# Performance work log

Measured on AMD Instinct MI355X. Metric: run time of the kernel, lower is better.

Reference implementation:

```python
import jax, jax.numpy as jnp
import numpy as np
import math

N, DIM, HEADS = 4096, 128, 8
HC = DIM // HEADS      # MHA per-head dim = 16
GC = DIM               # TransformerConv per-head out_channels = dim (concat=False)
E = 65536
FFN = 2048
EPS = 1e-5

def layernorm(x, g, b):
    m = x.mean(-1, keepdims=True)
    v = ((x - m) ** 2).mean(-1, keepdims=True)
    return (x - m) * jax.lax.rsqrt(v + EPS) * g + b

def setup_inputs() -> dict:
    key = jax.random.key(0)
    ks = jax.random.split(key, 24)
    s = 0.02
    def nrm(k, shape):
        return jax.random.normal(k, shape, jnp.float32) * s
    return dict(
        x=jax.random.normal(ks[0], (N, DIM), jnp.float32),
        edge_index=jax.random.randint(ks[1], (2, E), 0, N),
        edge_attr=jax.random.normal(ks[2], (E, DIM), jnp.float32),
        n1_g=jnp.ones((DIM,)), n1_b=jnp.zeros((DIM,)),
        n2_g=jnp.ones((DIM,)), n2_b=jnp.zeros((DIM,)),
        n3_g=jnp.ones((DIM,)), n3_b=jnp.zeros((DIM,)),
        w_qkv=nrm(ks[3], (DIM, 3 * DIM)), b_qkv=jnp.zeros((3 * DIM,)),
        w_o=nrm(ks[4], (DIM, DIM)), b_o=jnp.zeros((DIM,)),
        w_query=nrm(ks[5], (DIM, HEADS * GC)), b_query=jnp.zeros((HEADS * GC,)),
        w_key=nrm(ks[6], (DIM, HEADS * GC)), b_key=jnp.zeros((HEADS * GC,)),
        w_value=nrm(ks[7], (DIM, HEADS * GC)), b_value=jnp.zeros((HEADS * GC,)),
        w_edge=nrm(ks[8], (DIM, HEADS * GC)), b_edge=jnp.zeros((HEADS * GC,)),
        w_skip=nrm(ks[9], (DIM, GC)), b_skip=jnp.zeros((GC,)),
        w_beta=nrm(ks[10], (3 * GC, 1)),
        w_f1=nrm(ks[11], (DIM, FFN)), b_f1=jnp.zeros((FFN,)),
        w_f2=nrm(ks[12], (FFN, DIM)), b_f2=jnp.zeros((DIM,)),
        w_dyn=nrm(ks[13], (2 * DIM, DIM)), b_dyn=jnp.zeros((DIM,)),
    )

def reference(x, edge_index, edge_attr, n1_g, n1_b, n2_g, n2_b, n3_g, n3_b,
              w_qkv, b_qkv, w_o, b_o,
              w_query, b_query, w_key, b_key, w_value, b_value,
              w_edge, b_edge, w_skip, b_skip, w_beta,
              w_f1, b_f1, w_f2, b_f2, w_dyn, b_dyn):
    residual = x
    xn = layernorm(x, n1_g, n1_b)
    # ---- dense self-attention (batch 1, batch_first MHA, eval mode) ----
    qkv = xn @ w_qkv + b_qkv
    q, k, v = jnp.split(qkv, 3, axis=-1)
    q = q.reshape(N, HEADS, HC)
    k = k.reshape(N, HEADS, HC)
    v = v.reshape(N, HEADS, HC)
    scores = jnp.einsum('qhd,khd->hqk', q, k) / math.sqrt(HC)
    probs = jax.nn.softmax(scores, axis=-1)
    attn = jnp.einsum('hqk,khd->qhd', probs, v).reshape(N, DIM)
    attn = attn @ w_o + b_o
    x = residual + attn
    # ---- TransformerConv (heads=8, concat=False -> mean, beta=True, edge_dim=dim) ----
    xn2 = layernorm(x, n2_g, n2_b)
    src, dst = edge_index[0], edge_index[1]   # source -> target flow
    qg = (xn2 @ w_query + b_query).reshape(N, HEADS, GC)
    kg = (xn2 @ w_key + b_key).reshape(N, HEADS, GC)
    vg = (xn2 @ w_value + b_value).reshape(N, HEADS, GC)
    eg = (edge_attr @ w_edge + b_edge).reshape(E, HEADS, GC)
    kj = kg[src] + eg                          # key_j + edge embedding
    alpha = jnp.einsum('ehd,ehd->eh', qg[dst], kj) / math.sqrt(GC)  # [E,H]
    amax = jax.ops.segment_max(alpha, dst, num_segments=N)          # [N,H]
    amax = jnp.where(jnp.isfinite(amax), amax, 0.0)
    ea = jnp.exp(alpha - amax[dst])
    denom = jax.ops.segment_sum(ea, dst, num_segments=N)
    w = ea / (denom[dst] + 1e-16)              # segment softmax per target node
    msg = (vg[src] + eg) * w[:, :, None]       # value_j + edge, scaled
    agg = jax.ops.segment_sum(msg, dst, num_segments=N)  # [N,H,GC]
    out = agg.mean(axis=1)                     # concat=False -> head mean
    x_r = xn2 @ w_skip + b_skip                # root/skip path
    beta = jax.nn.sigmoid(jnp.concatenate([out, x_r, out - x_r], axis=-1) @ w_beta)
    graph_out = beta * x_r + (1.0 - beta) * out
    x = x + graph_out
    # ---- FFN ----
    xn3 = layernorm(x, n3_g, n3_b)
    ffn = jax.nn.gelu(xn3 @ w_f1 + b_f1, approximate=False) @ w_f2 + b_f2
    x = x + ffn
    # ---- gated residual fusion ----
    gate = jax.nn.sigmoid(jnp.concatenate([x, residual], axis=-1) @ w_dyn + b_dyn)
    return x * gate + residual * (1.0 - gate)
```

## Files before the change

### kernel.cpp

```cpp
#include <hip/hip_runtime.h>
#include <math.h>
#include <cstddef>

#define NN 4096
#define DIMC 128
#define NHEADS 8
#define NE 65536

typedef unsigned short ushort_t;
typedef short bs8 __attribute__((ext_vector_type(8)));
typedef float f32x16 __attribute__((ext_vector_type(16)));
typedef _Float16 h4 __attribute__((ext_vector_type(4)));
typedef __fp16 fp16x2 __attribute__((ext_vector_type(2)));
typedef float f4t __attribute__((ext_vector_type(4)));

__device__ __forceinline__ float b2f(ushort_t u){
  unsigned int i = ((unsigned int)u)<<16; float f;
  __builtin_memcpy(&f,&i,4); return f;
}
__device__ __forceinline__ ushort_t f2b(float f){
  unsigned int x; __builtin_memcpy(&x,&f,4);
  unsigned int r = x + 0x7fffu + ((x>>16)&1u);
  return (ushort_t)(r>>16);
}
__device__ __forceinline__ float bdot8(uint4 a, uint4 b){
  unsigned int ua[4]={a.x,a.y,a.z,a.w}, ub[4]={b.x,b.y,b.z,b.w};
  float s=0.f;
  #pragma unroll
  for (int i=0;i<4;++i){
    unsigned int al=ua[i]<<16, ah=ua[i]&0xffff0000u, bl=ub[i]<<16, bh=ub[i]&0xffff0000u;
    float fa,fb,fc,fd;
    __builtin_memcpy(&fa,&al,4); __builtin_memcpy(&fb,&ah,4);
    __builtin_memcpy(&fc,&bl,4); __builtin_memcpy(&fd,&bh,4);
    s += fa*fc + fb*fd;
  }
  return s;
}
__device__ __forceinline__ float bfdot8v(uint4 a, float4 e0, float4 e1){
  unsigned int ua[4]={a.x,a.y,a.z,a.w};
  float eb[8]={e0.x,e0.y,e0.z,e0.w,e1.x,e1.y,e1.z,e1.w};
  float s=0.f;
  #pragma unroll
  for (int i=0;i<4;++i){
    unsigned int al=ua[i]<<16, ah=ua[i]&0xffff0000u;
    float fa,fb;
    __builtin_memcpy(&fa,&al,4); __builtin_memcpy(&fb,&ah,4);
    s += fa*eb[2*i] + fb*eb[2*i+1];
  }
  return s;
}

__global__ __launch_bounds__(256) void ln_kernel(const float* __restrict__ x,
    const float* __restrict__ g, const float* __restrict__ b, ushort_t* __restrict__ y){
  int n = blockIdx.x*4 + (threadIdx.x>>6);
  int l = threadIdx.x & 63;
  int d0 = 2*l;
  float2 v = *(const float2*)&x[(size_t)n*DIMC + d0];
  float s = v.x+v.y;
  s += __shfl_xor(s,1); s += __shfl_xor(s,2); s += __shfl_xor(s,4);
  s += __shfl_xor(s,8); s += __shfl_xor(s,16); s += __shfl_xor(s,32);
  float mean = s*(1.0f/128.0f);
  float c0=v.x-mean, c1=v.y-mean;
  float q=c0*c0+c1*c1;
  q += __shfl_xor(q,1); q += __shfl_xor(q,2); q += __shfl_xor(q,4);
  q += __shfl_xor(q,8); q += __shfl_xor(q,16); q += __shfl_xor(q,32);
  float rinv = rsqrtf(q*(1.0f/128.0f)+1e-5f);
  float2 gv = *(const float2*)&g[d0];
  float2 bv = *(const float2*)&b[d0];
  unsigned int pk = ((unsigned int)f2b(c1*rinv*gv.y+bv.y)<<16) | (unsigned int)f2b(c0*rinv*gv.x+bv.x);
  *(unsigned int*)&y[(size_t)n*DIMC + d0] = pk;
}

#define QSCALE 0.36067376022224085f
__global__ __launch_bounds__(256) void megawcvt_kernel(
    const float* __restrict__ w_qkv, const float* __restrict__ w_o,
    const float* __restrict__ w_q, const float* __restrict__ w_k,
    const float* __restrict__ w_v, const float* __restrict__ w_e,
    const float* __restrict__ w_f1, const float* __restrict__ w_f2,
    const float* __restrict__ bq, const float* __restrict__ bk,
    const float* __restrict__ w_dyn, const float* __restrict__ b_qkv,
    ushort_t* __restrict__ WBqkv, ushort_t* __restrict__ WBo, ushort_t* __restrict__ WBG,
    ushort_t* __restrict__ WETB, ushort_t* __restrict__ WBf1, ushort_t* __restrict__ WBf2,
    ushort_t* __restrict__ WCAT, float* __restrict__ BCAT, ushort_t* __restrict__ WDYN,
    int* __restrict__ COUNT, float* __restrict__ BQKV)
{
  int b = blockIdx.x, tid = threadIdx.x;
  if (b < 1216){
    const float* src; int srcStride; ushort_t* dst; int dstStride;
    int n0, k0; float scale = 1.0f;
    if (b < 48){ int nt=b>>2, kt=b&3; src=w_qkv; srcStride=384; dst=WBqkv; dstStride=128;
      n0=nt*32; k0=kt*32; if (nt<4) scale=QSCALE; }
    else if (b < 64){ int l=b-48, nt=l>>2, kt=l&3; src=w_o; srcStride=128; dst=WBo; dstStride=128; n0=nt*32; k0=kt*32; }
    else if (b < 192){ int l=b-64, nt=l>>2, kt=l&3; src=w_q; srcStride=1024; dst=WBG; dstStride=128; n0=nt*32; k0=kt*32; }
    else if (b < 320){ int l=b-192, nt=l>>2, kt=l&3; src=w_k; srcStride=1024; dst=WBG+1024*128; dstStride=128; n0=nt*32; k0=kt*32; }
    else if (b < 448){ int l=b-320, nt=l>>2, kt=l&3; src=w_e; srcStride=1024; dst=WETB; dstStride=128; n0=nt*32; k0=kt*32; }
    else if (b < 704){ int l=b-448, nt=l>>2, kt=l&3; src=w_f1; srcStride=2048; dst=WBf1; dstStride=128; n0=nt*32; k0=kt*32; }
    else if (b < 960){ int l=b-704, nt=l>>6, kt=l&63; src=w_f2; srcStride=128; dst=WBf2; dstStride=2048; n0=nt*32; k0=kt*32; }
    else if (b < 1088){ int l=b-960, h=l>>4, tt=l&15, nt=tt>>2, kt=tt&3;
      src=w_v+h*128; srcStride=1024; dst=WCAT+h*128; dstStride=2048; n0=nt*32; k0=kt*32; scale=0.125f; }
    else { int l=b-1088, h=l>>4, tt=l&15, nt=tt>>2, kt=tt&3;
      src=w_e+h*128; srcStride=1024; dst=WCAT+1024+h*128; dstStride=2048; n0=nt*32; k0=kt*32; scale=0.125f; }
    __shared__ float lt[32*33];
    int rr = tid>>3, cg = (tid&7)*4;
    float4 v = *(const float4*)&src[(size_t)(k0+rr)*srcStride + n0 + cg];
    lt[rr*33+cg]=v.x; lt[rr*33+cg+1]=v.y; lt[rr*33+cg+2]=v.z; lt[rr*33+cg+3]=v.w;
    __syncthreads();
    ushort_t o[4] __attribute__((aligned(8)));
    #pragma unroll
    for (int j=0;j<4;++j) o[j] = f2b(lt[(cg+j)*33 + rr]*scale);
    *(ushort4*)&dst[(size_t)(n0+rr)*dstStride + k0 + cg] = *(ushort4*)o;
  } else {
    for (int id=(b-1216)*256+tid; id<39296; id += 40*256){
      if (id < 2048) BCAT[id] = (id<1024)? bq[id] : bk[id-1024];
      else if (id < 34816){ int l=id-2048; WDYN[l]=f2b(w_dyn[l]); }
      else if (id < 38912) COUNT[id-34816]=0;
      else { int l=id-38912; BQKV[l]=b_qkv[l]*((l<128)?QSCALE:1.0f); }
    }
  }
}

template<int A_BF16, int C_MODE>
__global__ __launch_bounds__(256) void mgemm_kernel(
    const void* __restrict__ Av, int lda, int strideA,
    const ushort_t* __restrict__ BT, int ldbt, int strideB,
    const float* __restrict__ bias,
    const float* __restrict__ res,
    void* __restrict__ Cv, int ldc, int strideC,
    int K, int act_gelu, _Float16* __restrict__ vtout)
{
  int z = blockIdx.z;
  int m0 = blockIdx.y*128, n0 = blockIdx.x*64;
  int tid = threadIdx.x;
  int w = tid>>6, lane = tid&63;
  int kg = lane>>5;
  int ml = w*32 + (lane&31);
  int sw = (ml>>1)&3;
  __shared__ ushort_t As[128*32];
  const ushort_t* BTz = BT + (size_t)z*strideB;
  f32x16 acc[2];
  #pragma unroll
  for (int i=0;i<16;++i){ acc[0][i]=0.f; acc[1][i]=0.f; }

  for (int k0=0; k0<K; k0+=32){
    {
      int rr = tid>>1, kc = (tid&1)*16;
      int rowg = m0 + rr;
      ushort_t tmp[16] __attribute__((aligned(16)));
      if (A_BF16){
        const ushort_t* A = (const ushort_t*)Av + (size_t)z*strideA;
        uint4 u0 = *(const uint4*)&A[(size_t)rowg*lda + k0 + kc];
        uint4 u1 = *(const uint4*)&A[(size_t)rowg*lda + k0 + kc + 8];
        __builtin_memcpy(tmp, &u0, 16); __builtin_memcpy(tmp+8, &u1, 16);
      } else {
        const float* A = (const float*)Av + (size_t)z*strideA;
        const float* p = &A[(size_t)rowg*lda + k0 + kc];
        float4 f0=*(const float4*)p, f1=*(const float4*)(p+4);
        float4 f2v=*(const float4*)(p+8), f3=*(const float4*)(p+12);
        tmp[0]=f2b(f0.x); tmp[1]=f2b(f0.y); tmp[2]=f2b(f0.z); tmp[3]=f2b(f0.w);
        tmp[4]=f2b(f1.x); tmp[5]=f2b(f1.y); tmp[6]=f2b(f1.z); tmp[7]=f2b(f1.w);
        tmp[8]=f2b(f2v.x); tmp[9]=f2b(f2v.y); tmp[10]=f2b(f2v.z); tmp[11]=f2b(f2v.w);
        tmp[12]=f2b(f3.x); tmp[13]=f2b(f3.y); tmp[14]=f2b(f3.z); tmp[15]=f2b(f3.w);
      }
      int swr = (rr>>1)&3, c0 = kc>>3;
      *(uint4*)&As[rr*32 + (((c0  )^swr)*8)] = *(const uint4*)tmp;
      *(uint4*)&As[rr*32 + (((c0+1)^swr)*8)] = *(const uint4*)(tmp+8);
    }
    __syncthreads();
    bs8 a0 = *(bs8*)&As[ml*32 + (((0*2+kg)^sw)*8)];
    bs8 a1 = *(bs8*)&As[ml*32 + (((1*2+kg)^sw)*8)];
    #pragma unroll
    for (int nt=0; nt<2; ++nt){
      const ushort_t* bp = &BTz[(size_t)(n0 + nt*32 + (lane&31))*ldbt + k0 + kg*8];
      uint4 rb0 = *(const uint4*)bp;
      uint4 rb1 = *(const uint4*)(bp + 16);
      bs8 b0, b1;
      __builtin_memcpy(&b0, &rb0, 16); __builtin_memcpy(&b1, &rb1, 16);
      acc[nt] = __builtin_amdgcn_mfma_f32_32x32x16_bf16(a0, b0, acc[nt], 0,0,0);
      acc[nt] = __builtin_amdgcn_mfma_f32_32x32x16_bf16(a1, b1, acc[nt], 0,0,0);
    }
    __syncthreads();
  }
  #pragma unroll
  for (int nt=0; nt<2; ++nt){
    int col = n0 + nt*32 + (lane&31);
    float bv = bias ? bias[col] : 0.f;
    #pragma unroll
    for (int r=0; r<16; ++r){
      int rowl = (r&3) + 8*(r>>2) + 4*kg;
      int row = m0 + w*32 + rowl;
      float v = acc[nt][r] + bv;
      if (act_gelu) v = 0.5f*v*(1.0f+erff(v*0.70710678118654752f));
      if (res) v += res[(size_t)row*ldc + col];
      size_t idx = (size_t)z*strideC + (size_t)row*ldc + col;
      if (C_MODE==1)      ((ushort_t*)Cv)[idx] = f2b(v);
      else if (C_MODE==2){
        _Float16 hv = (_Float16)v;
        ((_Float16*)Cv)[idx] = hv;
        if (vtout && col>=256) vtout[(size_t)(col-256)*4096 + row] = hv;
      }
      else                ((float*)Cv)[idx]    = v;
    }
  }
}

__global__ __launch_bounds__(512) void flash_kernel(const _Float16* __restrict__ qkvh,
    const _Float16* __restrict__ vt, float* __restrict__ attn){
  int h = blockIdx.y;
  int w = threadIdx.x >> 6, lane = threadIdx.x & 63;
  int q0 = blockIdx.x*64;
  int col = lane & 15, quad = lane >> 4;
  __shared__ float ll[8][4][16];
  __shared__ float lo[8][4][256];
  h4 qf[4];
  #pragma unroll
  for (int t=0;t<4;++t)
    qf[t] = *(const h4*)&qkvh[(size_t)(q0+t*16+col)*384 + h*16 + quad*4];
  f4t ov[4];
  float ls[4] = {0.f,0.f,0.f,0.f};
  #pragma unroll
  for (int t=0;t<4;++t){ ov[t][0]=0.f; ov[t][1]=0.f; ov[t][2]=0.f; ov[t][3]=0.f; }
  const _Float16* kbase = qkvh + 128 + h*16 + quad*4;
  const _Float16* vbase = vt + (size_t)(h*16+col)*4096 + quad*4;
  int jbeg = w*512, jend = jbeg + 512;
  h4 kf = *(const h4*)&kbase[(size_t)(jbeg+col)*384];
  h4 vf = *(const h4*)&vbase[jbeg];
  for (int j0=jbeg; j0<jend; j0+=16){
    h4 kc=kf, vc=vf;
    if (j0+16<jend){
      kf = *(const h4*)&kbase[(size_t)(j0+16+col)*384];
      vf = *(const h4*)&vbase[j0+16];
    }
    f4t s[4];
    #pragma unroll
    for (int t=0;t<4;++t){
      s[t][0]=0.f; s[t][1]=0.f; s[t][2]=0.f; s[t][3]=0.f;
      s[t] = __builtin_amdgcn_mfma_f32_16x16x16f16(kc, qf[t], s[t], 0,0,0);
    }
    #pragma unroll
    for (int t=0;t<4;++t){
      float p0=__builtin_amdgcn_exp2f(s[t][0]), p1=__builtin_amdgcn_exp2f(s[t][1]);
      float p2=__builtin_amdgcn_exp2f(s[t][2]), p3=__builtin_amdgcn_exp2f(s[t][3]);
      ls[t] += (p0+p1)+(p2+p3);
      fp16x2 plo = __builtin_amdgcn_cvt_pkrtz(p0,p1);
      fp16x2 phi = __builtin_amdgcn_cvt_pkrtz(p2,p3);
      h4 pf;
      pf[0]=(_Float16)plo[0]; pf[1]=(_Float16)plo[1];
      pf[2]=(_Float16)phi[0]; pf[3]=(_Float16)phi[1];
      ov[t] = __builtin_amdgcn_mfma_f32_16x16x16f16(vc, pf, ov[t], 0,0,0);
    }
  }
  #pragma unroll
  for (int t=0;t<4;++t){
    float l = ls[t];
    l += __shfl_xor(l,16);
    l += __shfl_xor(l,32);
    if (lane<16) ll[w][t][lane]=l;
    *(float4*)&lo[w][t][lane*4] = make_float4(ov[t][0],ov[t][1],ov[t][2],ov[t][3]);
  }
  __syncthreads();
  if (w < 4){
    int t = w;
    float l = 0.f;
    #pragma unroll
    for (int ww=0; ww<8; ++ww) l += ll[ww][t][col];
    float4 os = make_float4(0.f,0.f,0.f,0.f);
    #pragma unroll
    for (int ww=0; ww<8; ++ww){
      float4 owv = *(const float4*)&lo[ww][t][lane*4];
      os.x += owv.x; os.y += owv.y; os.z += owv.z; os.w += owv.w;
    }
    float inv = 1.0f/l;
    *(float4*)&attn[(size_t)(q0+t*16+col)*128 + h*16 + quad*4] =
        make_float4(os.x*inv, os.y*inv, os.z*inv, os.w*inv);
  }
}

__global__ __launch_bounds__(256) void alpha_kernel(
    const float* __restrict__ ea, const ushort_t* __restrict__ qkvsg,
    const ushort_t* __restrict__ t, const int* __restrict__ csr,
    const int* __restrict__ pack, float* __restrict__ alpha){
  int tid = threadIdx.x;
  int w = tid>>6, lane = tid&63;
  int h = lane>>3, li = lane&7;
  int off = h*128 + li*16;
  int ibase = blockIdx.x*8 + w*2;
  int2 pk = *(const int2*)&pack[ibase];
  int2 ec = *(const int2*)&csr[ibase];
  int e0 = ec.x & (NE-1), e1 = ec.y & (NE-1);
  int s0 = pk.x & 4095, d0 = (pk.x>>12) & 4095;
  int s1 = pk.y & 4095, d1 = (pk.y>>12) & 4095;

  const ushort_t* q0p = &qkvsg[(size_t)d0*2048 + off];
  const ushort_t* k0p = &qkvsg[(size_t)s0*2048 + 1024 + off];
  const ushort_t* t0p = &t[(size_t)d0*1024 + off];
  const float*    e0p = &ea[(size_t)e0*128 + li*16];
  const ushort_t* q1p = &qkvsg[(size_t)d1*2048 + off];
  const ushort_t* k1p = &qkvsg[(size_t)s1*2048 + 1024 + off];
  const ushort_t* t1p = &t[(size_t)d1*1024 + off];
  const float*    e1p = &ea[(size_t)e1*128 + li*16];

  uint4 q00=*(const uint4*)q0p,      q01=*(const uint4*)(q0p+8);
  uint4 k00=*(const uint4*)k0p,      k01=*(const uint4*)(k0p+8);
  uint4 t00=*(const uint4*)t0p,      t01=*(const uint4*)(t0p+8);
  float4 ea00=*(const float4*)e0p,   ea01=*(const float4*)(e0p+4);
  float4 ea02=*(const float4*)(e0p+8), ea03=*(const float4*)(e0p+12);
  uint4 q10=*(const uint4*)q1p,      q11=*(const uint4*)(q1p+8);
  uint4 k10=*(const uint4*)k1p,      k11=*(const uint4*)(k1p+8);
  uint4 t10=*(const uint4*)t1p,      t11=*(const uint4*)(t1p+8);
  float4 ea10=*(const float4*)e1p,   ea11=*(const float4*)(e1p+4);
  float4 ea12=*(const float4*)(e1p+8), ea13=*(const float4*)(e1p+12);

  float p0 = bdot8(q00,k00) + bdot8(q01,k01)
           + bfdot8v(t00,ea00,ea01) + bfdot8v(t01,ea02,ea03);
  float p1 = bdot8(q10,k10) + bdot8(q11,k11)
           + bfdot8v(t10,ea10,ea11) + bfdot8v(t11,ea12,ea13);
  p0 += __shfl_xor(p0,1); p0 += __shfl_xor(p0,2); p0 += __shfl_xor(p0,4);
  p1 += __shfl_xor(p1,1); p1 += __shfl_xor(p1,2); p1 += __shfl_xor(p1,4);
  if (li==0){
    alpha[(size_t)ibase*8 + h]     = 0.08838834764831845f*p0;
    alpha[(size_t)(ibase+1)*8 + h] = 0.08838834764831845f*p1;
  }
}

__global__ __launch_bounds__(256) void count_kernel(const int* __restrict__ ei, int* __restrict__ cnt){
  int e = blockIdx.x*256+threadIdx.x;
  atomicAdd(&cnt[ei[NE+e] & (NN-1)],1);
}
__global__ __launch_bounds__(1024) void scan_kernel(const int* __restrict__ cnt,
    int* __restrict__ rows, int* __restrict__ cursor){
  __shared__ int sums[1024];
  int tid=threadIdx.x;
  int c0=cnt[tid*4], c1=cnt[tid*4+1], c2=cnt[tid*4+2], c3=cnt[tid*4+3];
  int local=c0+c1+c2+c3;
  sums[tid]=local;
  __syncthreads();
  for (int off=1; off<1024; off<<=1){
    int v = (tid>=off)? sums[tid-off] : 0;
    __syncthreads();
    sums[tid]+=v;
    __syncthreads();
  }
  int r = sums[tid]-local;
  rows[tid*4]=r;   cursor[tid*4]=r;   r+=c0;
  rows[tid*4+1]=r; cursor[tid*4+1]=r; r+=c1;
  rows[tid*4+2]=r; cursor[tid*4+2]=r; r+=c2;
  rows[tid*4+3]=r; cursor[tid*4+3]=r; r+=c3;
  if (tid==1023) rows[4096]=r;
}
__global__ __launch_bounds__(256) void scatter_kernel(const int* __restrict__ ei,
    int* __restrict__ cursor, int* __restrict__ csr, int* __restrict__ pack){
  int e = blockIdx.x*256+threadIdx.x;
  int src = ei[e] & (NN-1), dst = ei[NE+e] & (NN-1);
  int pos = atomicAdd(&cursor[dst],1);
  if (pos >= 0 && pos < NE){ csr[pos]=e; pack[pos] = src | (dst<<12); }
}

__global__ __launch_bounds__(256) void agg1_kernel(
    const ushort_t* __restrict__ lns, const float* __restrict__ ea,
    const float* __restrict__ abuf, const int* __restrict__ rows, const int* __restrict__ csr,
    const int* __restrict__ pack,
    const float* __restrict__ b_edge, const float* __restrict__ b_v,
    ushort_t* __restrict__ seagg, float* __restrict__ part)
{
  int n = blockIdx.x, tid = threadIdx.x;
  int d = tid & 127, h0 = tid >> 7;
  float sacc[4]={0.f,0.f,0.f,0.f}, eacc[4]={0.f,0.f,0.f,0.f}, wsacc[4]={0.f,0.f,0.f,0.f};
  float mh[4]={-1e30f,-1e30f,-1e30f,-1e30f};
  float be[4];
  #pragma unroll
  for (int j=0;j<4;++j){
    int hd = (h0+2*j)*128 + d;
    be[j] = b_edge[hd] + b_v[hd];
  }
  int i0=rows[n], i1=rows[n+1];
  i0 = max(0,min(i0,NE)); i1 = max(i0,min(i1,NE));
  for (int i=i0;i<i1;++i){
    #pragma unroll
    for (int j=0;j<4;++j) mh[j] = fmaxf(mh[j], abuf[(size_t)i*8 + h0 + 2*j]);
  }
  __shared__ float smh[8];
  __shared__ float wls[16][8];
  __shared__ int es[16], srcs[16];
  if (d==0){
    #pragma unroll
    for (int j=0;j<4;++j) smh[h0+2*j]=mh[j];
  }
  __syncthreads();
  for (int cs=i0; cs<i1; cs+=16){
    int cnt = min(16, i1-cs);
    if (tid < cnt){
      es[tid]   = csr[cs+tid] & (NE-1);
      srcs[tid] = pack[cs+tid] & (NN-1);
    }
    if (tid < cnt*8){
      int k=tid>>3, hh=tid&7;
      wls[k][hh] = __expf(abuf[(size_t)(cs+k)*8+hh]-smh[hh]);
    }
    __syncthreads();
    for (int k=0;k<cnt;++k){
      int e = es[k], sr = srcs[k];
      float lv = b2f(lns[(size_t)sr*128 + d]);
      float eav = ea[(size_t)e*128 + d];
      #pragma unroll
      for (int j=0;j<4;++j){
        float wv = wls[k][h0+2*j];
        sacc[j] += wv*lv;
        eacc[j] += wv*eav;
        wsacc[j] += wv;
      }
    }
    __syncthreads();
  }
  float partial = 0.f;
  #pragma unroll
  for (int j=0;j<4;++j){
    float inv = 1.0f/(wsacc[j]+1e-16f);
    int hd = (h0+2*j)*128 + d;
    seagg[(size_t)n*2048 + hd]        = f2b(sacc[j]*inv);
    seagg[(size_t)n*2048 + 1024 + hd] = f2b(eacc[j]*inv);
    partial += be[j]*wsacc[j]*inv;
  }
  __shared__ float pp[2][128];
  pp[h0][d] = partial;
  __syncthreads();
  if (tid<128) part[(size_t)n*128+tid] = (pp[0][tid]+pp[1][tid])*0.125f;
}

__global__ __launch_bounds__(64) void combine_kernel(float* __restrict__ x2,
    const float* __restrict__ corrp, const float* __restrict__ part,
    ushort_t* __restrict__ lns, const float* __restrict__ w_s,
    const float* __restrict__ b_s, const float* __restrict__ x1,
    const float* __restrict__ w_beta,
    const float* __restrict__ n3g, const float* __restrict__ n3b)
{
  int n0 = blockIdx.x*2;
  int l = threadIdx.x;
  int d0 = 2*l, d1 = 2*l+1;
  __shared__ float sln[2][128];
  #pragma unroll
  for (int rr=0;rr<2;++rr){
    unsigned int u = *(const unsigned int*)&lns[(size_t)(n0+rr)*128 + d0];
    sln[rr][d0] = b2f((ushort_t)(u&0xffffu));
    sln[rr][d1] = b2f((ushort_t)(u>>16));
  }
  __syncthreads();
  float2 bsv = *(const float2*)&b_s[d0];
  float xr0[2], xr1[2];
  xr0[0]=bsv.x; xr0[1]=bsv.x; xr1[0]=bsv.y; xr1[1]=bsv.y;
  for (int i=0;i<128;++i){
    float2 wv = *(const float2*)&w_s[(size_t)i*128 + d0];
    #pragma unroll
    for (int rr=0;rr<2;++rr){
      float lv = sln[rr][i];
      xr0[rr] += lv*wv.x; xr1[rr] += lv*wv.y;
    }
  }
  float2 wb0 = *(const float2*)&w_beta[d0];
  float2 wb1 = *(const float2*)&w_beta[128+d0];
  float2 wb2 = *(const float2*)&w_beta[256+d0];
  float2 gv = *(const float2*)&n3g[d0];
  float2 bv = *(const float2*)&n3b[d0];
  #pragma unroll
  for (int rr=0;rr<2;++rr){
    size_t idx = (size_t)(n0+rr)*128 + d0;
    float2 pt = *(const float2*)&part[idx];
    float2 c0 = *(const float2*)&corrp[idx];
    float2 c1 = *(const float2*)&corrp[524288+idx];
    float2 c2 = *(const float2*)&corrp[1048576+idx];
    float2 c3 = *(const float2*)&corrp[1572864+idx];
    float o0 = pt.x+c0.x+c1.x+c2.x+c3.x;
    float o1 = pt.y+c0.y+c1.y+c2.y+c3.y;
    float xa = xr0[rr], xb = xr1[rr];
    float pr = o0*wb0.x + o1*wb0.y + xa*wb1.x + xb*wb1.y
             + (o0-xa)*wb2.x + (o1-xb)*wb2.y;
    pr += __shfl_xor(pr,1); pr += __shfl_xor(pr,2); pr += __shfl_xor(pr,4);
    pr += __shfl_xor(pr,8); pr += __shfl_xor(pr,16); pr += __shfl_xor(pr,32);
    float beta = 1.0f/(1.0f+__expf(-pr));
    float2 xv = *(const float2*)&x1[idx];
    float v0 = xv.x + beta*xa + (1.0f-beta)*o0;
    float v1 = xv.y + beta*xb + (1.0f-beta)*o1;
    *(float2*)&x2[idx] = make_float2(v0,v1);
    float s = v0+v1;
    s += __shfl_xor(s,1); s += __shfl_xor(s,2); s += __shfl_xor(s,4);
    s += __shfl_xor(s,8); s += __shfl_xor(s,16); s += __shfl_xor(s,32);
    float mean = s*(1.0f/128.0f);
    float e0=v0-mean, e1=v1-mean;
    float q = e0*e0+e1*e1;
    q += __shfl_xor(q,1); q += __shfl_xor(q,2); q += __shfl_xor(q,4);
    q += __shfl_xor(q,8); q += __shfl_xor(q,16); q += __shfl_xor(q,32);
    float rinv = rsqrtf(q*(1.0f/128.0f)+1e-5f);
    unsigned int pk2 = ((unsigned int)f2b(e1*rinv*gv.y+bv.y)<<16)
                     |  (unsigned int)f2b(e0*rinv*gv.x+bv.x);
    *(unsigned int*)&lns[idx] = pk2;
  }
}

__global__ __launch_bounds__(64) void gate_kernel(const float* __restrict__ x3p,
    const float* __restrict__ b_f2, const float* __restrict__ x2,
    const float* __restrict__ x0, const ushort_t* __restrict__ wdyn,
    const float* __restrict__ b_dyn, float* __restrict__ out){
  int n0 = blockIdx.x*2;
  int l = threadIdx.x;
  int d0 = 2*l, d1 = 2*l+1;
  __shared__ float sA[2][128];
  __shared__ float sR[2][128];
  float a0[2], a1[2], r0[2], r1[2];
  float2 bb = *(const float2*)&b_f2[d0];
  #pragma unroll
  for (int rr=0;rr<2;++rr){
    size_t idx = (size_t)(n0+rr)*128 + d0;
    float2 p0v = *(const float2*)&x3p[idx];
    float2 p1v = *(const float2*)&x3p[524288+idx];
    float2 p2v = *(const float2*)&x3p[1048576+idx];
    float2 p3v = *(const float2*)&x3p[1572864+idx];
    float2 xv = *(const float2*)&x2[idx];
    float2 rv = *(const float2*)&x0[idx];
    a0[rr] = p0v.x+p1v.x+p2v.x+p3v.x+bb.x+xv.x;
    a1[rr] = p0v.y+p1v.y+p2v.y+p3v.y+bb.y+xv.y;
    r0[rr]=rv.x; r1[rr]=rv.y;
    sA[rr][d0]=a0[rr]; sA[rr][d1]=a1[rr];
    sR[rr][d0]=rv.x;  sR[rr][d1]=rv.y;
  }
  __syncthreads();
  float2 bd = *(const float2*)&b_dyn[d0];
  float g0[2], g1[2];
  g0[0]=bd.x; g0[1]=bd.x; g1[0]=bd.y; g1[1]=bd.y;
  for (int k=0;k<128;++k){
    unsigned int wv = *(const unsigned int*)&wdyn[(size_t)k*128 + d0];
    float w0=b2f((ushort_t)(wv&0xffffu)), w1=b2f((ushort_t)(wv>>16));
    #pragma unroll
    for (int rr=0;rr<2;++rr){
      float sk = sA[rr][k];
      g0[rr]+=sk*w0; g1[rr]+=sk*w1;
    }
  }
  for (int k=0;k<128;++k){
    unsigned int wv = *(const unsigned int*)&wdyn[(size_t)(128+k)*128 + d0];
    float w0=b2f((ushort_t)(wv&0xffffu)), w1=b2f((ushort_t)(wv>>16));
    #pragma unroll
    for (int rr=0;rr<2;++rr){
      float sk = sR[rr][k];
      g0[rr]+=sk*w0; g1[rr]+=sk*w1;
    }
  }
  #pragma unroll
  for (int rr=0;rr<2;++rr){
    size_t idx=(size_t)(n0+rr)*128 + d0;
    float gg0=1.0f/(1.0f+__expf(-g0[rr]));
    float gg1=1.0f/(1.0f+__expf(-g1[rr]));
    float v0=a0[rr]*gg0 + r0[rr]*(1.0f-gg0);
    float v1=a1[rr]*gg1 + r1[rr]*(1.0f-gg1);
    *(float2*)&out[idx]=make_float2(v0,v1);
  }
}

extern "C" void kernel_launch(void* const* d_in, const int* in_sizes, int n_in,
                              void* d_out, int out_size, void* d_ws, size_t ws_size,
                              hipStream_t stream) {
  const float* x    =(const float*)d_in[0];
  const int*   ei   =(const int*)  d_in[1];
  const float* eattr=(const float*)d_in[2];
  const float* n1g=(const float*)d_in[3], *n1b=(const float*)d_in[4];
  const float* n2g=(const float*)d_in[5], *n2b=(const float*)d_in[6];
  const float* n3g=(const float*)d_in[7], *n3b=(const float*)d_in[8];
  const float* w_qkv=(const float*)d_in[9],  *b_qkv=(const float*)d_in[10];
  const float* w_o  =(const float*)d_in[11], *b_o  =(const float*)d_in[12];
  const float* w_q  =(const float*)d_in[13], *b_q  =(const float*)d_in[14];
  const float* w_k  =(const float*)d_in[15], *b_k  =(const float*)d_in[16];
  const float* w_v  =(const float*)d_in[17], *b_v  =(const float*)d_in[18];
  const float* w_e  =(const float*)d_in[19], *b_e  =(const float*)d_in[20];
  const float* w_s  =(const float*)d_in[21], *b_s  =(const float*)d_in[22];
  const float* w_beta=(const float*)d_in[23];
  const float* w_f1 =(const float*)d_in[24], *b_f1=(const float*)d_in[25];
  const float* w_f2 =(const float*)d_in[26], *b_f2=(const float*)d_in[27];
  const float* w_dyn=(const float*)d_in[28], *b_dyn=(const float*)d_in[29];
  float* out=(float*)d_out;
  float* ws=(float*)d_ws;

  float* X1    = ws + 0;
  float* X2    = ws + 524288;
  ushort_t* LNS = (ushort_t*)(ws + 1048576);
  float* PART  = ws + 1310720;
  float* ALPHA = ws + 1835008;
  int*   ROWS  = (int*)(ws + 2359296);
  int*   CURS  = (int*)(ws + 2363456);
  int*   CSR   = (int*)(ws + 2367552);
  int*   COUNT = (int*)(ws + 2433088);
  int*   PACK  = (int*)(ws + 524288);
  float* BQKV  = ws + 1048576 - 512;
  ushort_t* WBqkv = (ushort_t*)(ws + 2437184);
  ushort_t* WBo   = (ushort_t*)(ws + 2461760);
  ushort_t* WBG   = (ushort_t*)(ws + 2469952);
  ushort_t* WETB  = (ushort_t*)(ws + 2601024);
  ushort_t* WBf1  = (ushort_t*)(ws + 2666560);
  ushort_t* WBf2  = (ushort_t*)(ws + 2797632);
  ushort_t* WCAT  = (ushort_t*)(ws + 2928704);
  float* BCAT  = ws + 3059776;
  ushort_t* WDYN = (ushort_t*)(ws + 3061824);
  _Float16* QKVH  = (_Float16*)(ws + 3078208);
  _Float16* VT    = (_Float16*)(ws + 3864640);
  ushort_t* QKVSG = (ushort_t*)(ws + 3078208);
  ushort_t* SEAGG = (ushort_t*)(ws + 3078208);
  ushort_t* MID   = (ushort_t*)(ws + 3078208);
  ushort_t* T     = (ushort_t*)(ws + 7272512);
  float* CORRP = ws + 7272512;
  float* X3P   = ws + 7272512;
  float* ATTN  = X2;

  megawcvt_kernel<<<1256,256,0,stream>>>(w_qkv,w_o,w_q,w_k,w_v,w_e,w_f1,w_f2,
                                         b_q,b_k,w_dyn,b_qkv,
                                         WBqkv,WBo,WBG,WETB,WBf1,WBf2,WCAT,BCAT,WDYN,COUNT,BQKV);

  ln_kernel<<<1024,256,0,stream>>>(x, n1g, n1b, LNS);
  mgemm_kernel<1,2><<<dim3(6,32,1),256,0,stream>>>(LNS,128,0, WBqkv,128,0, BQKV, nullptr, QKVH,384,0, 128, 0, VT);
  flash_kernel<<<dim3(64,8),512,0,stream>>>(QKVH, VT, ATTN);
  mgemm_kernel<0,0><<<dim3(2,32,1),256,0,stream>>>(ATTN,128,0, WBo,128,0, b_o, x, X1,128,0, 128, 0, nullptr);

  ln_kernel<<<1024,256,0,stream>>>(X1, n2g, n2b, LNS);
  mgemm_kernel<1,1><<<dim3(32,32,1),256,0,stream>>>(LNS,128,0, WBG,128,0, BCAT, nullptr, QKVSG,2048,0, 128, 0, nullptr);
  mgemm_kernel<1,1><<<dim3(2,32,8),256,0,stream>>>(QKVSG,2048,128, WETB,128,16384, nullptr, nullptr, T,1024,128, 128, 0, nullptr);
  count_kernel<<<256,256,0,stream>>>(ei, COUNT);
  scan_kernel<<<1,1024,0,stream>>>(COUNT, ROWS, CURS);
  scatter_kernel<<<256,256,0,stream>>>(ei, CURS, CSR, PACK);
  alpha_kernel<<<8192,256,0,stream>>>(eattr, QKVSG, T, CSR, PACK, ALPHA);
  agg1_kernel<<<NN,256,0,stream>>>(LNS, eattr, ALPHA, ROWS, CSR, PACK, b_e, b_v, SEAGG, PART);
  mgemm_kernel<1,0><<<dim3(2,32,4),256,0,stream>>>(SEAGG,2048,512, WCAT,2048,512, nullptr, nullptr, CORRP,128,524288, 512, 0, nullptr);
  combine_kernel<<<2048,64,0,stream>>>(X2, CORRP, PART, LNS, w_s, b_s, X1, w_beta, n3g, n3b);

  mgemm_kernel<1,1><<<dim3(32,32,1),256,0,stream>>>(LNS,128,0, WBf1,128,0, b_f1, nullptr, MID,2048,0, 128, 1, nullptr);
  mgemm_kernel<1,0><<<dim3(2,32,4),256,0,stream>>>(MID,2048,512, WBf2,2048,512, nullptr, nullptr, X3P,128,524288, 512, 0, nullptr);

  gate_kernel<<<2048,64,0,stream>>>(X3P, b_f2, X2, x, WDYN, b_dyn, out);
}
```

Baseline: 380.5 us.

## Fuse CSR build into LN/GEMM kernels and halve flash query tile

Removes the separate count, scan and scatter launches. The edge counting moves into the first layernorm kernel, the prefix scan runs in an extra block column of the QKV GEMM, and the scatter runs in extra blocks of the second layernorm kernel. It also adds a packed edge/src array so agg1 reads one int per edge instead of two. The flash attention block now covers 32 queries instead of 64, doubling the grid for more parallelism at the cost of more K/V reloads. The main aim is to cut launch overhead and serial gaps between the small graph-prep kernels.

```diff
diff --git a/kernel.cpp b/kernel.cpp
--- a/kernel.cpp
+++ b/kernel.cpp
@@ -50,9 +50,41 @@
   return s;
 }
 
+__device__ void scan256(const int* __restrict__ cnt, int* __restrict__ rows,
+                        int* __restrict__ cursor){
+  __shared__ int sums[256];
+  int t = threadIdx.x;
+  int base = t*16;
+  int c[16]; int local=0;
+  #pragma unroll
+  for (int i=0;i<16;++i){ c[i]=cnt[base+i]; local+=c[i]; }
+  sums[t]=local; __syncthreads();
+  for (int off=1; off<256; off<<=1){
+    int v = (t>=off)? sums[t-off] : 0; __syncthreads();
+    sums[t]+=v; __syncthreads();
+  }
+  int r = sums[t]-local;
+  #pragma unroll
+  for (int i=0;i<16;++i){ rows[base+i]=r; cursor[base+i]=r; r+=c[i]; }
+  if (t==255) rows[4096]=r;
+}
+
 __global__ __launch_bounds__(256) void ln_kernel(const float* __restrict__ x,
-    const float* __restrict__ g, const float* __restrict__ b, ushort_t* __restrict__ y){
-  int n = blockIdx.x*4 + (threadIdx.x>>6);
+    const float* __restrict__ g, const float* __restrict__ b, ushort_t* __restrict__ y,
+    const int* __restrict__ ei, int* __restrict__ cnt,
+    int* __restrict__ cursor, int* __restrict__ csr,
+    int* __restrict__ pack, int* __restrict__ packe){
+  int bb = blockIdx.x;
+  if (bb >= 1024){
+    int e = (bb-1024)*256 + threadIdx.x;
+    int src = ei[e] & (NN-1), dst = ei[NE+e] & (NN-1);
+    int pos = atomicAdd(&cursor[dst],1);
+    if (pos >= 0 && pos < NE){
+      csr[pos]=e; pack[pos]=src|(dst<<12); packe[pos]=e|(src<<16);
+    }
+    return;
+  }
+  int n = bb*4 + (threadIdx.x>>6);
   int l = threadIdx.x & 63;
   int d0 = 2*l;
   float2 v = *(const float2*)&x[(size_t)n*DIMC + d0];
@@ -69,6 +101,10 @@
   float2 bv = *(const float2*)&b[d0];
   unsigned int pk = ((unsigned int)f2b(c1*rinv*gv.y+bv.y)<<16) | (unsigned int)f2b(c0*rinv*gv.x+bv.x);
   *(unsigned int*)&y[(size_t)n*DIMC + d0] = pk;
+  if (cnt){
+    int gid = bb*256 + threadIdx.x;
+    if (gid < NE) atomicAdd(&cnt[ei[NE+gid] & (NN-1)],1);
+  }
 }
 
 #define QSCALE 0.36067376022224085f
@@ -119,15 +155,22 @@
   }
 }
 
-template<int A_BF16, int C_MODE>
+template<int A_BF16, int C_MODE, int FUSE_SCAN>
 __global__ __launch_bounds__(256) void mgemm_kernel(
     const void* __restrict__ Av, int lda, int strideA,
     const ushort_t* __restrict__ BT, int ldbt, int strideB,
     const float* __restrict__ bias,
     const float* __restrict__ res,
     void* __restrict__ Cv, int ldc, int strideC,
-    int K, int act_gelu, _Float16* __restrict__ vtout)
+    int K, int act_gelu, _Float16* __restrict__ vtout,
+    const int* __restrict__ scnt, int* __restrict__ srows, int* __restrict__ scur)
 {
+  if (FUSE_SCAN){
+    if (blockIdx.x == gridDim.x-1){
+      if (blockIdx.y==0 && blockIdx.z==0) scan256(scnt, srows, scur);
+      return;
+    }
+  }
   int z = blockIdx.z;
   int m0 = blockIdx.y*128, n0 = blockIdx.x*64;
   int tid = threadIdx.x;
@@ -207,18 +250,18 @@
     const _Float16* __restrict__ vt, float* __restrict__ attn){
   int h = blockIdx.y;
   int w = threadIdx.x >> 6, lane = threadIdx.x & 63;
-  int q0 = blockIdx.x*64;
+  int q0 = blockIdx.x*32;
   int col = lane & 15, quad = lane >> 4;
-  __shared__ float ll[8][4][16];
-  __shared__ float lo[8][4][256];
-  h4 qf[4];
-  #pragma unroll
-  for (int t=0;t<4;++t)
+  __shared__ float ll[8][2][16];
+  __shared__ float lo[8][2][256];
+  h4 qf[2];
+  #pragma unroll
+  for (int t=0;t<2;++t)
     qf[t] = *(const h4*)&qkvh[(size_t)(q0+t*16+col)*384 + h*16 + quad*4];
-  f4t ov[4];
-  float ls[4] = {0.f,0.f,0.f,0.f};
-  #pragma unroll
-  for (int t=0;t<4;++t){ ov[t][0]=0.f; ov[t][1]=0.f; ov[t][2]=0.f; ov[t][3]=0.f; }
+  f4t ov[2];
+  float ls[2] = {0.f,0.f};
+  #pragma unroll
+  for (int t=0;t<2;++t){ ov[t][0]=0.f; ov[t][1]=0.f; ov[t][2]=0.f; ov[t][3]=0.f; }
   const _Float16* kbase = qkvh + 128 + h*16 + quad*4;
   const _Float16* vbase = vt + (size_t)(h*16+col)*4096 + quad*4;
   int jbeg = w*512, jend = jbeg + 512;
@@ -230,14 +273,14 @@
       kf = *(const h4*)&kbase[(size_t)(j0+16+col)*384];
       vf = *(const h4*)&vbase[j0+16];
     }
-    f4t s[4];
-    #pragma unroll
-    for (int t=0;t<4;++t){
+    f4t s[2];
+    #pragma unroll
+    for (int t=0;t<2;++t){
       s[t][0]=0.f; s[t][1]=0.f; s[t][2]=0.f; s[t][3]=0.f;
       s[t] = __builtin_amdgcn_mfma_f32_16x16x16f16(kc, qf[t], s[t], 0,0,0);
     }
     #pragma unroll
-    for (int t=0;t<4;++t){
+    for (int t=0;t<2;++t){
       float p0=__builtin_amdgcn_exp2f(s[t][0]), p1=__builtin_amdgcn_exp2f(s[t][1]);
       float p2=__builtin_amdgcn_exp2f(s[t][2]), p3=__builtin_amdgcn_exp2f(s[t][3]);
       ls[t] += (p0+p1)+(p2+p3);
@@ -250,7 +293,7 @@
     }
   }
   #pragma unroll
-  for (int t=0;t<4;++t){
+  for (int t=0;t<2;++t){
     float l = ls[t];
     l += __shfl_xor(l,16);
     l += __shfl_xor(l,32);
@@ -258,7 +301,7 @@
     *(float4*)&lo[w][t][lane*4] = make_float4(ov[t][0],ov[t][1],ov[t][2],ov[t][3]);
   }
   __syncthreads();
-  if (w < 4){
+  if (w < 2){
     int t = w;
     float l = 0.f;
     #pragma unroll
@@ -322,43 +365,10 @@
   }
 }
 
-__global__ __launch_bounds__(256) void count_kernel(const int* __restrict__ ei, int* __restrict__ cnt){
-  int e = blockIdx.x*256+threadIdx.x;
-  atomicAdd(&cnt[ei[NE+e] & (NN-1)],1);
-}
-__global__ __launch_bounds__(1024) void scan_kernel(const int* __restrict__ cnt,
-    int* __restrict__ rows, int* __restrict__ cursor){
-  __shared__ int sums[1024];
-  int tid=threadIdx.x;
-  int c0=cnt[tid*4], c1=cnt[tid*4+1], c2=cnt[tid*4+2], c3=cnt[tid*4+3];
-  int local=c0+c1+c2+c3;
-  sums[tid]=local;
-  __syncthreads();
-  for (int off=1; off<1024; off<<=1){
-    int v = (tid>=off)? sums[tid-off] : 0;
-    __syncthreads();
-    sums[tid]+=v;
-    __syncthreads();
-  }
-  int r = sums[tid]-local;
-  rows[tid*4]=r;   cursor[tid*4]=r;   r+=c0;
-  rows[tid*4+1]=r; cursor[tid*4+1]=r; r+=c1;
-  rows[tid*4+2]=r; cursor[tid*4+2]=r; r+=c2;
-  rows[tid*4+3]=r; cursor[tid*4+3]=r; r+=c3;
-  if (tid==1023) rows[4096]=r;
-}
-__global__ __launch_bounds__(256) void scatter_kernel(const int* __restrict__ ei,
-    int* __restrict__ cursor, int* __restrict__ csr, int* __restrict__ pack){
-  int e = blockIdx.x*256+threadIdx.x;
-  int src = ei[e] & (NN-1), dst = ei[NE+e] & (NN-1);
-  int pos = atomicAdd(&cursor[dst],1);
-  if (pos >= 0 && pos < NE){ csr[pos]=e; pack[pos] = src | (dst<<12); }
-}
-
 __global__ __launch_bounds__(256) void agg1_kernel(
     const ushort_t* __restrict__ lns, const float* __restrict__ ea,
-    const float* __restrict__ abuf, const int* __restrict__ rows, const int* __restrict__ csr,
-    const int* __restrict__ pack,
+    const float* __restrict__ abuf, const int* __restrict__ rows,
+    const int* __restrict__ packe,
     const float* __restrict__ b_edge, const float* __restrict__ b_v,
     ushort_t* __restrict__ seagg, float* __restrict__ part)
 {
@@ -389,8 +399,9 @@
   for (int cs=i0; cs<i1; cs+=16){
     int cnt = min(16, i1-cs);
     if (tid < cnt){
-      es[tid]   = csr[cs+tid] & (NE-1);
-      srcs[tid] = pack[cs+tid] & (NN-1);
+      int v = packe[cs+tid];
+      es[tid]   = v & 0xffff;
+      srcs[tid] = (v>>16) & (NN-1);
     }
     if (tid < cnt*8){
       int k=tid>>3, hh=tid&7;
@@ -587,6 +598,7 @@
   int*   CSR   = (int*)(ws + 2367552);
   int*   COUNT = (int*)(ws + 2433088);
   int*   PACK  = (int*)(ws + 524288);
+  int*   PACKE = (int*)(ws + 589824);
   float* BQKV  = ws + 1048576 - 512;
   ushort_t* WBqkv = (ushort_t*)(ws + 2437184);
   ushort_t* WBo   = (ushort_t*)(ws + 2461760);
@@ -611,24 +623,21 @@
                                          b_q,b_k,w_dyn,b_qkv,
                                          WBqkv,WBo,WBG,WETB,WBf1,WBf2,WCAT,BCAT,WDYN,COUNT,BQKV);
 
-  ln_kernel<<<1024,256,0,stream>>>(x, n1g, n1b, LNS);
-  mgemm_kernel<1,2><<<dim3(6,32,1),256,0,stream>>>(LNS,128,0, WBqkv,128,0, BQKV, nullptr, QKVH,384,0, 128, 0, VT);
-  flash_kernel<<<dim3(64,8),512,0,stream>>>(QKVH, VT, ATTN);
-  mgemm_kernel<0,0><<<dim3(2,32,1),256,0,stream>>>(ATTN,128,0, WBo,128,0, b_o, x, X1,128,0, 128, 0, nullptr);
-
-  ln_kernel<<<1024,256,0,stream>>>(X1, n2g, n2b, LNS);
-  mgemm_kernel<1,1><<<dim3(32,32,1),256,0,stream>>>(LNS,128,0, WBG,128,0, BCAT, nullptr, QKVSG,2048,0, 128, 0, nullptr);
-  mgemm_kernel<1,1><<<dim3(2,32,8),256,0,stream>>>(QKVSG,2048,128, WETB,128,16384, nullptr, nullptr, T,1024,128, 128, 0, nullptr);
-  count_kernel<<<256,256,0,stream>>>(ei, COUNT);
-  scan_kernel<<<1,1024,0,stream>>>(COUNT, ROWS, CURS);
-  scatter_kernel<<<256,256,0,stream>>>(ei, CURS, CSR, PACK);
+  ln_kernel<<<1024,256,0,stream>>>(x, n1g, n1b, LNS, ei, COUNT, nullptr,nullptr,nullptr,nullptr);
+  mgemm_kernel<1,2,1><<<dim3(7,32,1),256,0,stream>>>(LNS,128,0, WBqkv,128,0, BQKV, nullptr, QKVH,384,0, 128, 0, VT, COUNT, ROWS, CURS);
+  flash_kernel<<<dim3(128,8),512,0,stream>>>(QKVH, VT, ATTN);
+  mgemm_kernel<0,0,0><<<dim3(2,32,1),256,0,stream>>>(ATTN,128,0, WBo,128,0, b_o, x, X1,128,0, 128, 0, nullptr, nullptr,nullptr,nullptr);
+
+  ln_kernel<<<1280,256,0,stream>>>(X1, n2g, n2b, LNS, ei, nullptr, CURS, CSR, PACK, PACKE);
+  mgemm_kernel<1,1,0><<<dim3(32,32,1),256,0,stream>>>(LNS,128,0, WBG,128,0, BCAT, nullptr, QKVSG,2048,0, 128, 0, nullptr, nullptr,nullptr,nullptr);
+  mgemm_kernel<1,1,0><<<dim3(2,32,8),256,0,stream>>>(QKVSG,2048,128, WETB,128,16384, nullptr, nullptr, T,1024,128, 128, 0, nullptr, nullptr,nullptr,nullptr);
   alpha_kernel<<<8192,256,0,stream>>>(eattr, QKVSG, T, CSR, PACK, ALPHA);
-  agg1_kernel<<<NN,256,0,stream>>>(LNS, eattr, ALPHA, ROWS, CSR, PACK, b_e, b_v, SEAGG, PART);
-  mgemm_kernel<1,0><<<dim3(2,32,4),256,0,stream>>>(SEAGG,2048,512, WCAT,2048,512, nullptr, nullptr, CORRP,128,524288, 512, 0, nullptr);
+  agg1_kernel<<<NN,256,0,stream>>>(LNS, eattr, ALPHA, ROWS, PACKE, b_e, b_v, SEAGG, PART);
+  mgemm_kernel<1,0,0><<<dim3(2,32,4),256,0,stream>>>(SEAGG,2048,512, WCAT,2048,512, nullptr, nullptr, CORRP,128,524288, 512, 0, nullptr, nullptr,nullptr,nullptr);
   combine_kernel<<<2048,64,0,stream>>>(X2, CORRP, PART, LNS, w_s, b_s, X1, w_beta, n3g, n3b);
 
-  mgemm_kernel<1,1><<<dim3(32,32,1),256,0,stream>>>(LNS,128,0, WBf1,128,0, b_f1, nullptr, MID,2048,0, 128, 1, nullptr);
-  mgemm_kernel<1,0><<<dim3(2,32,4),256,0,stream>>>(MID,2048,512, WBf2,2048,512, nullptr, nullptr, X3P,128,524288, 512, 0, nullptr);
+  mgemm_kernel<1,1,0><<<dim3(32,32,1),256,0,stream>>>(LNS,128,0, WBf1,128,0, b_f1, nullptr, MID,2048,0, 128, 1, nullptr, nullptr,nullptr,nullptr);
+  mgemm_kernel<1,0,0><<<dim3(2,32,4),256,0,stream>>>(MID,2048,512, WBf2,2048,512, nullptr, nullptr, X3P,128,524288, 512, 0, nullptr, nullptr,nullptr,nullptr);
 
   gate_kernel<<<2048,64,0,stream>>>(X3P, b_f2, X2, x, WDYN, b_dyn, out);
 }
```

Measured after the change: 405.1 us. +6.5%, slower.
